# Kernel optimization log

Measured on AMD Instinct MI355X. Metric: run time of the kernel, lower is better.

Reference implementation:

```python
import jax, jax.numpy as jnp
import numpy as np
from jax import lax

WS = 7          # window size
SHIFT = 3       # shift size
HEADS = 16
DIM = 512
NREF = 100
H_IMG = 112
W_IMG = 112
BATCH = 2
HD = DIM // HEADS
SCALE = HD ** (-0.5)
EPS = 1e-5


def _layernorm(x, w, b):
    mu = jnp.mean(x, axis=-1, keepdims=True)
    var = jnp.mean((x - mu) ** 2, axis=-1, keepdims=True)
    return (x - mu) / jnp.sqrt(var + EPS) * w + b


def _rel_pos_index():
    coords = np.stack(np.meshgrid(np.arange(WS), np.arange(WS), indexing='ij'))  # (2,ws,ws)
    cf = coords.reshape(2, -1)
    rel = cf[:, :, None] - cf[:, None, :]
    rel = rel.transpose(1, 2, 0).astype(np.int64)
    rel[..., 0] += WS - 1
    rel[..., 1] += WS - 1
    rel[..., 0] *= 2 * WS - 1
    return rel.sum(-1).reshape(-1)  # (N*N,)

_RPI = _rel_pos_index()


def setup_inputs() -> dict:
    key = jax.random.key(0)
    ks = jax.random.split(key, 16)
    C = DIM
    s = 0.02
    x = jax.random.normal(ks[0], (BATCH, H_IMG * W_IMG, C), jnp.float32)
    x_ref = jax.random.normal(ks[1], (BATCH, NREF, C), jnp.float32)
    # shifted-window attention mask (standard Swin construction)
    img = np.zeros((H_IMG, W_IMG))
    cnt = 0
    for hs in (slice(0, -WS), slice(-WS, -SHIFT), slice(-SHIFT, None)):
        for ws_ in (slice(0, -WS), slice(-WS, -SHIFT), slice(-SHIFT, None)):
            img[hs, ws_] = cnt
            cnt += 1
    mw = img.reshape(H_IMG // WS, WS, W_IMG // WS, WS).transpose(0, 2, 1, 3).reshape(-1, WS * WS)
    am = mw[:, None, :] - mw[:, :, None]
    mask = jnp.asarray(np.where(am != 0, -100.0, 0.0), jnp.float32)  # (nW, N, N)
    return dict(
        x=x, x_ref=x_ref, mask=mask,
        norm1_w=jnp.ones((C,), jnp.float32), norm1_b=jnp.zeros((C,), jnp.float32),
        qkv_w=jax.random.normal(ks[2], (3 * C, C), jnp.float32) * s,
        qkv_b=jnp.zeros((3 * C,), jnp.float32),
        diff_mu=jax.random.normal(ks[3], (1, 1, C), jnp.float32),
        diff_logsigma=jax.random.normal(ks[4], (1, 1, C), jnp.float32) * s,
        rpb_table=jax.random.normal(ks[5], ((2 * WS - 1) ** 2, HEADS), jnp.float32) * s,
        ref_qk_w=jax.random.normal(ks[6], (2 * C, C), jnp.float32) * s,
        ref_qk_b=jnp.zeros((2 * C,), jnp.float32),
        conv_w=jax.random.normal(ks[7], (HEADS, HEADS, 3, 3), jnp.float32) * s,
        conv_b=jnp.zeros((HEADS,), jnp.float32),
        proj_w=jax.random.normal(ks[8], (C, C), jnp.float32) * s,
        proj_b=jnp.zeros((C,), jnp.float32),
        norm2_w=jnp.ones((C,), jnp.float32), norm2_b=jnp.zeros((C,), jnp.float32),
        fc1_w=jax.random.normal(ks[9], (4 * C, C), jnp.float32) * s,
        fc1_b=jnp.zeros((4 * C,), jnp.float32),
        fc2_w=jax.random.normal(ks[10], (C, 4 * C), jnp.float32) * s,
        fc2_b=jnp.zeros((C,), jnp.float32),
        Hh=H_IMG, Ww=W_IMG,
    )


def _window_attention(xw, mask, x_ref, qkv_w, qkv_b, diff_mu, diff_logsigma,
                      rpb_table, ref_qk_w, ref_qk_b, conv_w, conv_b, proj_w, proj_b):
    B_, N, C = xw.shape
    rB = x_ref.shape[0]
    n_win = B_ // rB
    qkv = (xw @ qkv_w.T + qkv_b).reshape(B_, N, 3, HEADS, HD).transpose(2, 0, 3, 1, 4)
    q, k, v = qkv[0], qkv[1], qkv[2]  # (B_, heads, N, hd)
    # reference tokens -> q/v with reparameterized shift/scale
    ref_qk = (x_ref @ ref_qk_w.T + ref_qk_b).reshape(rB, NREF, 2, C).transpose(2, 0, 1, 3)
    ref_q = diff_mu + jnp.exp(diff_logsigma) * ref_qk[0]
    ref_q = ref_q.reshape(rB, NREF, HEADS, HD).transpose(0, 2, 1, 3)
    ref_v = ref_qk[1].reshape(rB, NREF, HEADS, HD).transpose(0, 2, 1, 3)
    ref_k = jnp.repeat(ref_q, n_win, axis=0)  # (B_, heads, nref, hd)
    ref_v = jnp.repeat(ref_v, n_win, axis=0)
    ra = jnp.einsum('bhnd,bhrd->bhnr', q, ref_k)  # (B_, heads, N, nref)
    ra = ra.reshape(rB, n_win, HEADS, N, NREF).transpose(0, 2, 1, 3, 4).reshape(rB, HEADS, n_win * N, NREF)
    # 3 rounds of conv diffusion + layernorm(no affine) + gelu, residual
    for _ in range(3):
        u = lax.conv_general_dilated(ra, conv_w, (1, 1), 'SAME',
                                     dimension_numbers=('NCHW', 'OIHW', 'NCHW'))
        u = u + conv_b[None, :, None, None]
        mu = jnp.mean(u, axis=(-2, -1), keepdims=True)
        var = jnp.mean((u - mu) ** 2, axis=(-2, -1), keepdims=True)
        u = jax.nn.gelu((u - mu) / jnp.sqrt(var + EPS), approximate=False)
        ra = ra + u
    ra = ra.reshape(rB, HEADS, n_win, N, NREF).transpose(0, 2, 1, 3, 4).reshape(B_, HEADS, N, NREF)
    ra = jax.nn.softmax(ra, axis=-1)
    q_new = jnp.einsum('bhnr,bhrd->bhnd', ra, ref_v) * SCALE
    attn = jnp.einsum('bhnd,bhmd->bhnm', q_new, k)
    rpb = rpb_table[_RPI].reshape(N, N, HEADS).transpose(2, 0, 1)  # (heads, N, N)
    attn = attn + rpb[None]
    nW = mask.shape[0]
    attn = attn.reshape(B_ // nW, nW, HEADS, N, N) + mask[None, :, None]
    attn = jax.nn.softmax(attn.reshape(B_, HEADS, N, N), axis=-1)
    out = jnp.einsum('bhnm,bhmd->bhnd', attn, v).transpose(0, 2, 1, 3).reshape(B_, N, C)
    return out @ proj_w.T + proj_b


def reference(x, x_ref, mask, norm1_w, norm1_b, qkv_w, qkv_b, diff_mu, diff_logsigma,
              rpb_table, ref_qk_w, ref_qk_b, conv_w, conv_b, proj_w, proj_b,
              norm2_w, norm2_b, fc1_w, fc1_b, fc2_w, fc2_b, Hh, Ww):
    B, L, C = x.shape
    shortcut = x
    xn = _layernorm(x, norm1_w, norm1_b).reshape(B, Hh, Ww, C)
    # cyclic shift
    sx = jnp.roll(xn, (-SHIFT, -SHIFT), axis=(1, 2))
    # window partition -> (B*nWin, ws*ws, C)
    xw = sx.reshape(B, Hh // WS, WS, Ww // WS, WS, C).transpose(0, 1, 3, 2, 4, 5).reshape(-1, WS * WS, C)
    aw = _window_attention(xw, mask, x_ref, qkv_w, qkv_b, diff_mu, diff_logsigma,
                           rpb_table, ref_qk_w, ref_qk_b, conv_w, conv_b, proj_w, proj_b)
    # window reverse
    sx = aw.reshape(B, Hh // WS, Ww // WS, WS, WS, C).transpose(0, 1, 3, 2, 4, 5).reshape(B, Hh, Ww, C)
    xn = jnp.roll(sx, (SHIFT, SHIFT), axis=(1, 2)).reshape(B, L, C)
    x = shortcut + xn
    h = _layernorm(x, norm2_w, norm2_b)
    h = jax.nn.gelu(h @ fc1_w.T + fc1_b, approximate=False)
    return x + (h @ fc2_w.T + fc2_b)
```

## Files before the change

kernel.cpp:

```cpp
#include <hip/hip_runtime.h>
#include <hip/hip_bf16.h>

typedef __attribute__((ext_vector_type(8))) short short8;
typedef __attribute__((ext_vector_type(8))) unsigned short ushort8;
typedef __attribute__((ext_vector_type(4))) float f32x4;
typedef __attribute__((ext_vector_type(4))) unsigned int u32x4;
typedef __attribute__((ext_vector_type(2))) unsigned int u32x2;

#define DEV __device__ __forceinline__

DEV float gelu_f(float x) { return 0.5f * x * (1.f + erff(x * 0.70710678118654752440f)); }

DEV float bf2f(unsigned short s) {
  unsigned int t = ((unsigned int)s) << 16;
  float f; __builtin_memcpy(&f, &t, 4); return f;
}
DEV unsigned short f2bf(float f) {
  __hip_bfloat16 b = __float2bfloat16(f);
  unsigned short s; __builtin_memcpy(&s, &b, 2); return s;
}

DEV void async_copy16(void* lds, const void* g) {
  __builtin_amdgcn_global_load_lds(
      (const __attribute__((address_space(1))) unsigned int*)g,
      (__attribute__((address_space(3))) unsigned int*)lds, 16, 0, 0);
}

DEV void block_reduce2(float& s, float& s2) {
  __shared__ float red[8];
  int tid = threadIdx.x;
#pragma unroll
  for (int o = 32; o > 0; o >>= 1) { s += __shfl_down(s, o); s2 += __shfl_down(s2, o); }
  if ((tid & 63) == 0) { red[tid >> 6] = s; red[4 + (tid >> 6)] = s2; }
  __syncthreads();
  s  = red[0] + red[1] + red[2] + red[3];
  s2 = red[4] + red[5] + red[6] + red[7];
}

__global__ __launch_bounds__(256) void f2b_all_kernel(
    const float* __restrict__ qkv_w, const float* __restrict__ proj_w,
    const float* __restrict__ fc1_w, const float* __restrict__ fc2_w,
    __hip_bfloat16* __restrict__ wq, __hip_bfloat16* __restrict__ wp,
    __hip_bfloat16* __restrict__ w1, __hip_bfloat16* __restrict__ w2) {
  int i = blockIdx.x * 256 + threadIdx.x;
  const float* src; unsigned short* dst; int o;
  if (i < 98304)       { src = qkv_w;  dst = (unsigned short*)wq; o = i; }
  else if (i < 131072) { src = proj_w; dst = (unsigned short*)wp; o = i - 98304; }
  else if (i < 262144) { src = fc1_w;  dst = (unsigned short*)w1; o = i - 131072; }
  else                 { src = fc2_w;  dst = (unsigned short*)w2; o = i - 262144; }
  f32x4 a = *reinterpret_cast<const f32x4*>(&src[(size_t)o * 8]);
  f32x4 b = *reinterpret_cast<const f32x4*>(&src[(size_t)o * 8 + 4]);
  ushort8 v;
#pragma unroll
  for (int j = 0; j < 4; j++) { v[j] = f2bf(a[j]); v[4 + j] = f2bf(b[j]); }
  *reinterpret_cast<ushort8*>(&dst[(size_t)o * 8]) = v;
}

__global__ __launch_bounds__(256) void maskb_kernel(const float* __restrict__ mask,
                                                    unsigned short* __restrict__ maskB) {
  int i = blockIdx.x * 256 + threadIdx.x;
  int m = i % 56, rest = i / 56;
  int n = rest % 49, win = rest / 49;
  unsigned short v = 0;
  if (m < 49) v = f2bf(mask[((size_t)win * 49 + n) * 49 + m]);
  maskB[i] = v;
}

__global__ __launch_bounds__(256) void rpbt_kernel(const float* __restrict__ rpb,
                                                   unsigned short* __restrict__ rpbT) {
  int i = blockIdx.x * 256 + threadIdx.x;
  if (i >= 43904) return;
  int m = i % 56, rest = i / 56;
  int n = rest % 49, h = rest / 49;
  unsigned short v = 0;
  if (m < 49) {
    int rp = (n / 7 - m / 7 + 6) * 13 + (n % 7 - m % 7 + 6);
    v = f2bf(rpb[rp * 16 + h]);
  }
  rpbT[i] = v;
}

__global__ __launch_bounds__(256) void cwt_kernel(const float* __restrict__ cw,
                                                  unsigned short* __restrict__ cwT) {
  int i = blockIdx.x * 256 + threadIdx.x;
  if (i >= 2560) return;
  int co = i / 160, k = i % 160;
  unsigned short v = 0;
  if (k < 144) {
    int ci = k & 15, p = k >> 4;
    v = f2bf(cw[(co * 16 + ci) * 9 + p]);
  }
  cwT[i] = v;
}

__global__ __launch_bounds__(256) void ln1_window_kernel(
    const float* __restrict__ x, const float* __restrict__ w, const float* __restrict__ b,
    __hip_bfloat16* __restrict__ xw) {
  int tid = threadIdx.x;
  int wave = tid >> 6, lane = tid & 63;
  int t = blockIdx.x * 4 + wave;
  int b_ = t / 49, n = t % 49;
  int bb = b_ >> 8, win = b_ & 255;
  int wi = win >> 4, wj = win & 15;
  int ii = n / 7, jj = n % 7;
  int sh = (wi * 7 + ii + 3) % 112;
  int sw = (wj * 7 + jj + 3) % 112;
  const float* row = x + ((size_t)bb * 12544 + sh * 112 + sw) * 512;
  f32x4 v0 = *reinterpret_cast<const f32x4*>(&row[lane * 8]);
  f32x4 v1 = *reinterpret_cast<const f32x4*>(&row[lane * 8 + 4]);
  float s = 0.f, s2 = 0.f;
#pragma unroll
  for (int j = 0; j < 4; j++) {
    s += v0[j] + v1[j];
    s2 += v0[j] * v0[j] + v1[j] * v1[j];
  }
#pragma unroll
  for (int o = 1; o < 64; o <<= 1) { s += __shfl_xor(s, o); s2 += __shfl_xor(s2, o); }
  float mu = s * (1.f / 512.f);
  float rstd = rsqrtf(s2 * (1.f / 512.f) - mu * mu + 1e-5f);
  f32x4 w0 = *reinterpret_cast<const f32x4*>(&w[lane * 8]);
  f32x4 w1 = *reinterpret_cast<const f32x4*>(&w[lane * 8 + 4]);
  f32x4 c0 = *reinterpret_cast<const f32x4*>(&b[lane * 8]);
  f32x4 c1 = *reinterpret_cast<const f32x4*>(&b[lane * 8 + 4]);
  ushort8 o8;
#pragma unroll
  for (int j = 0; j < 4; j++) {
    o8[j]     = f2bf((v0[j] - mu) * rstd * w0[j] + c0[j]);
    o8[4 + j] = f2bf((v1[j] - mu) * rstd * w1[j] + c1[j]);
  }
  *reinterpret_cast<ushort8*>((unsigned short*)xw + (size_t)t * 512 + lane * 8) = o8;
}

template <int EPI>
__global__ __launch_bounds__(256, 6) void gemm_bt(
    const __hip_bfloat16* __restrict__ A, const __hip_bfloat16* __restrict__ B,
    const float* __restrict__ bias, float* __restrict__ outF,
    __hip_bfloat16* __restrict__ outB, int M, int N, int K) {
  __shared__ __align__(16) __hip_bfloat16 As[64 * 64];
  __shared__ __align__(16) __hip_bfloat16 Bs[128 * 64];
  int nn = N >> 7;
  int nblk = gridDim.x;
  int bid = blockIdx.x;
  int xcd = bid & 7, slot = bid >> 3;
  int q8 = nblk >> 3, r8 = nblk & 7;
  int base = xcd < r8 ? xcd * (q8 + 1) : r8 * (q8 + 1) + (xcd - r8) * q8;
  int lin = base + slot;
  int m0 = (lin / nn) << 6, n0 = (lin % nn) << 7;
  int tid = threadIdx.x;
  int wave = tid >> 6, lane = tid & 63;
  int wr = (wave >> 1) * 32, wc = (wave & 1) * 64;
  int lrow = lane & 15, kq = lane >> 4;
  int srow = lane >> 3, scol = (lane & 7) * 8;
  const __hip_bfloat16* Abase = A + (size_t)m0 * K;
  const __hip_bfloat16* Bbase = B + (size_t)n0 * K;
  f32x4 acc[2][4] = {};
  for (int k0 = 0; k0 < K; k0 += 64) {
#pragma unroll
    for (int i = 0; i < 2; i++) {
      int row = wave * 16 + i * 8;
      async_copy16(&As[row * 64], &Abase[(size_t)(row + srow) * K + k0 + scol]);
    }
#pragma unroll
    for (int i = 0; i < 4; i++) {
      int row = wave * 32 + i * 8;
      async_copy16(&Bs[row * 64], &Bbase[(size_t)(row + srow) * K + k0 + scol]);
    }
    __syncthreads();
#pragma unroll
    for (int ks = 0; ks < 2; ks++) {
      short8 af[2], bf[4];
#pragma unroll
      for (int t = 0; t < 2; t++)
        af[t] = *reinterpret_cast<const short8*>(&As[(wr + t * 16 + lrow) * 64 + ks * 32 + kq * 8]);
#pragma unroll
      for (int t = 0; t < 4; t++)
        bf[t] = *reinterpret_cast<const short8*>(&Bs[(wc + t * 16 + lrow) * 64 + ks * 32 + kq * 8]);
#pragma unroll
      for (int tm = 0; tm < 2; tm++)
#pragma unroll
        for (int tn = 0; tn < 4; tn++)
          acc[tm][tn] = __builtin_amdgcn_mfma_f32_16x16x32_bf16(af[tm], bf[tn], acc[tm][tn], 0, 0, 0);
    }
    __syncthreads();
  }
#pragma unroll
  for (int tm = 0; tm < 2; tm++) {
#pragma unroll
    for (int tn = 0; tn < 4; tn++) {
      int col = n0 + wc + tn * 16 + lrow;
      float bv = bias[col];
#pragma unroll
      for (int r = 0; r < 4; r++) {
        int row = m0 + wr + tm * 16 + kq * 4 + r;
        float v = acc[tm][tn][r] + bv;
        if (EPI == 4) {
          if (col < 512)
            ((unsigned short*)outB)[(size_t)row * 512 + col] = f2bf(v);
          else
            ((unsigned short*)outF)[(size_t)row * 1024 + (col - 512)] = f2bf(v);
        } else {
          size_t o = (size_t)row * N + col;
          if (EPI == 1) outB[o] = __float2bfloat16(v);
          else if (EPI == 2) outB[o] = __float2bfloat16(gelu_f(v));
          else outF[o] += v;
        }
      }
    }
  }
}

__global__ __launch_bounds__(256) void ref_kernel(
    const float* __restrict__ x_ref, const float* __restrict__ w, const float* __restrict__ bias,
    const float* __restrict__ diff_mu, const float* __restrict__ diff_ls,
    unsigned short* __restrict__ refq, unsigned short* __restrict__ refvT) {
  int blk = blockIdx.x;
  int b = blk / 100, r = blk % 100;
  __shared__ float xs[512];
  int tid = threadIdx.x;
  const float* xr = x_ref + (size_t)(b * 100 + r) * 512;
  xs[tid] = xr[tid];
  xs[tid + 256] = xr[tid + 256];
  __syncthreads();
#pragma unroll
  for (int cc = 0; cc < 4; cc++) {
    int c = cc * 256 + tid;
    const float* wr = w + (size_t)c * 512;
    float s = bias[c];
    for (int k = 0; k < 512; k++) s += xs[k] * wr[k];
    if (c < 512) {
      float v = diff_mu[c] + expf(diff_ls[c]) * s;
      int hh = c >> 5, d = c & 31;
      refq[((size_t)(b * 16 + hh) * 100 + r) * 32 + d] = f2bf(v);
    } else {
      int c2 = c - 512, hh = c2 >> 5, d = c2 & 31;
      refvT[(((size_t)b * 16 + hh) * 32 + d) * 128 + r] = f2bf(s);
    }
  }
  if (r < 28) {
#pragma unroll
    for (int j = 0; j < 2; j++) {
      int idx = j * 256 + tid;
      int hh = idx >> 5, d = idx & 31;
      refvT[(((size_t)b * 16 + hh) * 32 + d) * 128 + 100 + r] = 0;
    }
  }
}

__global__ __launch_bounds__(256) void ra_kernel(
    const __hip_bfloat16* __restrict__ q, const unsigned short* __restrict__ refq,
    __hip_bfloat16* __restrict__ ra) {
  __shared__ __align__(16) unsigned short q_s[64 * 40];
  __shared__ __align__(16) unsigned short rq_s[112 * 40];
  int bid = blockIdx.x;
  int blk = (bid & 7) * 1024 + (bid >> 3);
  int b_ = blk >> 4, h = blk & 15;
  int rb = b_ >> 8, win = b_ & 255;
  int tid = threadIdx.x;
  int wave = tid >> 6, lane = tid & 63;
  int lrow = lane & 15, kq = lane >> 4;
  u32x4 z4 = {};
  const unsigned short* qb = (const unsigned short*)q + (size_t)b_ * 49 * 512 + h * 32;
  for (int i = tid; i < 196; i += 256) {
    int n = i >> 2, c = i & 3;
    *reinterpret_cast<u32x4*>(&q_s[n * 40 + c * 8]) =
        *reinterpret_cast<const u32x4*>(&qb[n * 512 + c * 8]);
  }
  for (int i = tid; i < 60; i += 256) {
    int n = 49 + (i >> 2), c = i & 3;
    *reinterpret_cast<u32x4*>(&q_s[n * 40 + c * 8]) = z4;
  }
  const unsigned short* rqg = refq + (size_t)(rb * 16 + h) * 3200;
  for (int i = tid; i < 400; i += 256) {
    int r = i >> 2, c = i & 3;
    *reinterpret_cast<u32x4*>(&rq_s[r * 40 + c * 8]) =
        *reinterpret_cast<const u32x4*>(&rqg[r * 32 + c * 8]);
  }
  for (int i = tid; i < 48; i += 256) {
    int r = 100 + (i >> 2), c = i & 3;
    *reinterpret_cast<u32x4*>(&rq_s[r * 40 + c * 8]) = z4;
  }
  __syncthreads();
  short8 a = *reinterpret_cast<const short8*>(&q_s[(wave * 16 + lrow) * 40 + kq * 8]);
  unsigned short* ra_base = (unsigned short*)ra + ((size_t)(rb * 16 + h) * 12544 + win * 49) * 100;
  f32x4 zero = {};
#pragma unroll
  for (int nt = 0; nt < 7; nt++) {
    short8 b = *reinterpret_cast<const short8*>(&rq_s[(nt * 16 + lrow) * 40 + kq * 8]);
    f32x4 c = __builtin_amdgcn_mfma_f32_16x16x32_bf16(a, b, zero, 0, 0, 0);
    int col = nt * 16 + lrow;
#pragma unroll
    for (int r = 0; r < 4; r++) {
      int n = wave * 16 + kq * 4 + r;
      if (n < 49 && col < 100) ra_base[n * 100 + col] = f2bf(c[r]);
    }
  }
}

DEV int swzi(int pl, int ci) {
  int byte = (pl << 5) + (ci << 1);
  byte ^= ((pl >> 2) & 3) << 4;
  return byte >> 1;
}
__global__ __launch_bounds__(256, 6) void conv_kernel(
    const __hip_bfloat16* __restrict__ ra_, const unsigned short* __restrict__ cwT,
    const float* __restrict__ cb,
    __hip_bfloat16* __restrict__ u_, float* __restrict__ psum, float* __restrict__ psumsq) {
  __shared__ __align__(16) unsigned short in_s[6 * 103 * 16];
  __shared__ __align__(16) unsigned short st_s[4 * 16 * 36];
  __shared__ float sred_s[4][16], sred_s2[4][16];
  const unsigned short* ra = (const unsigned short*)ra_;
  unsigned short* u = (unsigned short*)u_;
  int ytb = blockIdx.x;
  int yt = (ytb & 7) * 392 + (ytb >> 3);
  int bb = blockIdx.y;
  int y0 = yt * 4;
  int tid = threadIdx.x;
  int wave = tid >> 6, lane = tid & 63;
  int lrow = lane & 15, kq = lane >> 4;
  for (int i = tid; i < 288; i += 256) {
    int ci = i & 15, rem = i >> 4;
    int yl = rem / 3, xs = rem % 3;
    int xl = (xs == 0) ? 0 : (100 + xs);
    in_s[swzi(yl * 103 + xl, ci)] = 0;
  }
  if (tid < 192) {
    int unit = tid >> 1, par = tid & 1;
    int ci = unit / 6, yl = unit % 6;
    int gy = y0 - 1 + yl;
    bool rv = (gy >= 0 && gy < 12544);
    const unsigned short* rp = ra + (((size_t)bb * 16 + ci) * 12544 + (rv ? gy : 0)) * 100;
    int plb = yl * 103 + 1;
#pragma unroll 4
    for (int c = par; c < 25; c += 2) {
      u32x2 d = {0u, 0u};
      if (rv) d = *reinterpret_cast<const u32x2*>(&rp[c * 4]);
      int pl = plb + c * 4;
      in_s[swzi(pl + 0, ci)] = (unsigned short)(d[0] & 0xffff);
      in_s[swzi(pl + 1, ci)] = (unsigned short)(d[0] >> 16);
      in_s[swzi(pl + 2, ci)] = (unsigned short)(d[1] & 0xffff);
      in_s[swzi(pl + 3, ci)] = (unsigned short)(d[1] >> 16);
    }
  }
  __syncthreads();

  short8 afr[5];
#pragma unroll
  for (int c = 0; c < 5; c++)
    afr[c] = *reinterpret_cast<const short8*>(&cwT[lrow * 160 + c * 32 + kq * 8]);
  int kqh = kq >> 1, ci0 = (kq & 1) * 8;
  int kyA[5], kxA[5];
#pragma unroll
  for (int c = 0; c < 5; c++) {
    int p = c * 2 + kqh; if (p > 8) p = 0;
    kyA[c] = p / 3; kxA[c] = p % 3;
  }
  float bias_r[4];
#pragma unroll
  for (int r = 0; r < 4; r++) bias_r[r] = cb[kq * 4 + r];
  float s_r[4] = {0.f, 0.f, 0.f, 0.f}, s2_r[4] = {0.f, 0.f, 0.f, 0.f};

  int yl = wave;
  int gy = y0 + yl;
  unsigned short* stw = &st_s[wave * 16 * 36];
  int seg = lane >> 2, part = lane & 3;
  const size_t ubase = ((size_t)bb * 16 * 12544 + gy) * 100;
#pragma unroll
  for (int xp = 0; xp < 4; xp++) {
#pragma unroll
    for (int xh = 0; xh < 2; xh++) {
      int xg = xp * 2 + xh;
      if (xg >= 7) break;
      int px = xg * 16 + lrow;
      int pxc = px < 100 ? px : 99;
      f32x4 acc = {};
#pragma unroll
      for (int c = 0; c < 5; c++) {
        short8 bfrag = *reinterpret_cast<const short8*>(
            &in_s[swzi((yl + kyA[c]) * 103 + pxc + kxA[c], ci0)]);
        acc = __builtin_amdgcn_mfma_f32_16x16x32_bf16(afr[c], bfrag, acc, 0, 0, 0);
      }
      bool valid = px < 100;
#pragma unroll
      for (int r = 0; r < 4; r++) {
        float v = acc[r] + bias_r[r];
        if (valid) {
          stw[(kq * 4 + r) * 36 + xh * 16 + lrow] = f2bf(v);
          s_r[r] += v; s2_r[r] += v * v;
        }
      }
    }
    unsigned short* ug = u + ubase + (size_t)seg * 1254400;
    if (xp < 3) {
      u32x2 d0 = *reinterpret_cast<const u32x2*>(&stw[seg * 36 + part * 4]);
      u32x2 d1 = *reinterpret_cast<const u32x2*>(&stw[seg * 36 + 16 + part * 4]);
      *reinterpret_cast<u32x2*>(&ug[xp * 32 + part * 4]) = d0;
      *reinterpret_cast<u32x2*>(&ug[xp * 32 + 16 + part * 4]) = d1;
    } else if (lane < 16) {
      u32x2 d = *reinterpret_cast<const u32x2*>(&st_s[wave * 16 * 36 + lane * 36]);
      *reinterpret_cast<u32x2*>(&u[ubase + (size_t)lane * 1254400 + 96]) = d;
    }
  }
#pragma unroll
  for (int o = 1; o < 16; o <<= 1)
#pragma unroll
    for (int r = 0; r < 4; r++) { s_r[r] += __shfl_xor(s_r[r], o); s2_r[r] += __shfl_xor(s2_r[r], o); }
  if (lrow == 0)
#pragma unroll
    for (int r = 0; r < 4; r++) { sred_s[wave][kq * 4 + r] = s_r[r]; sred_s2[wave][kq * 4 + r] = s2_r[r]; }
  __syncthreads();
  if (tid < 16) {
    float s  = sred_s[0][tid] + sred_s[1][tid] + sred_s[2][tid] + sred_s[3][tid];
    float s2 = sred_s2[0][tid] + sred_s2[1][tid] + sred_s2[2][tid] + sred_s2[3][tid];
    size_t pi = ((size_t)bb * 3136 + yt) * 16 + tid;
    psum[pi] = s; psumsq[pi] = s2;
  }
}

__global__ __launch_bounds__(256) void conv_stats_kernel(
    const float* __restrict__ psum, const float* __restrict__ psumsq, float* __restrict__ stats) {
  int g = blockIdx.x;
  int bb = g >> 4, co = g & 15;
  int tid = threadIdx.x;
  float s = 0.f, s2 = 0.f;
  for (int t = tid; t < 3136; t += 256) {
    size_t pi = ((size_t)bb * 3136 + t) * 16 + co;
    s += psum[pi];
    s2 += psumsq[pi];
  }
  block_reduce2(s, s2);
  if (tid == 0) {
    const float inv = 1.f / 1254400.f;
    float mu = s * inv;
    float var = s2 * inv - mu * mu;
    stats[g * 2] = mu;
    stats[g * 2 + 1] = rsqrtf(var + 1e-5f);
  }
}

__global__ __launch_bounds__(256) void conv_apply_kernel(
    __hip_bfloat16* __restrict__ ra, const __hip_bfloat16* __restrict__ u,
    const float* __restrict__ stats) {
  const int total8 = 5017600;
  int stride = gridDim.x * 256;
  for (int i = blockIdx.x * 256 + threadIdx.x; i < total8; i += stride) {
    int g = i / 156800;
    float mu = stats[g * 2], rstd = stats[g * 2 + 1];
    ushort8 uu = reinterpret_cast<const ushort8*>(u)[i];
    ushort8 rr = reinterpret_cast<const ushort8*>(ra)[i];
    ushort8 oo;
#pragma unroll
    for (int j = 0; j < 8; j++) {
      float rv = bf2f(rr[j]) + gelu_f((bf2f(uu[j]) - mu) * rstd);
      oo[j] = f2bf(rv);
    }
    reinterpret_cast<ushort8*>(ra)[i] = oo;
  }
}

template <int FUSE>
__global__ __launch_bounds__(256, 8) void attn_kernel(
    const __hip_bfloat16* __restrict__ ra_, const __hip_bfloat16* __restrict__ u_,
    const float* __restrict__ stats, const unsigned short* __restrict__ refvT,
    const __hip_bfloat16* __restrict__ kv_, const unsigned short* __restrict__ rpbT,
    const unsigned short* __restrict__ maskB, __hip_bfloat16* __restrict__ att_) {
  __shared__ __align__(16) char smem[18944];
  unsigned short* P1 = (unsigned short*)smem;
  unsigned short* P2 = (unsigned short*)smem;
  unsigned short* vT = (unsigned short*)(smem + 9216);
  unsigned short* qn = (unsigned short*)(smem + 13824);

#define LSUM(n) (*reinterpret_cast<float*>(&qn[(n) * 40 + 32]))

  int bid = blockIdx.x;
  int blk = (bid & 7) * 1024 + (bid >> 3);
  int b_ = blk >> 4, h = blk & 15;
  int rb = b_ >> 8, win = b_ & 255;
  int tid = threadIdx.x;
  int wave = tid >> 6, lane = tid & 63;
  int lrow = lane & 15, kq = lane >> 4;
  const unsigned short* ra = (const unsigned short*)ra_;
  const unsigned short* ug = (const unsigned short*)u_;
  const unsigned short* kv = (const unsigned short*)kv_;
  unsigned short* att = (unsigned short*)att_;
  u32x2 zz = {};

  if (tid < 64) LSUM(tid) = 1.0f;
  float mu = 0.f, rstd = 0.f;
  if (FUSE) { mu = stats[(rb * 16 + h) * 2]; rstd = stats[(rb * 16 + h) * 2 + 1]; }

  const size_t tile_off = ((size_t)(rb * 16 + h) * 12544 + win * 49) * 100;
  const unsigned short* rab = ra + tile_off;
  const unsigned short* uab = ug + tile_off;
  for (int i = tid; i < 1225; i += 256) {
    int n = i / 25, c = i % 25;
    u32x2 rv = *reinterpret_cast<const u32x2*>(&rab[n * 100 + c * 4]);
    if (FUSE) {
      u32x2 uv = *reinterpret_cast<const u32x2*>(&uab[n * 100 + c * 4]);
      unsigned short rr4[4] = {(unsigned short)(rv[0] & 0xffff), (unsigned short)(rv[0] >> 16),
                               (unsigned short)(rv[1] & 0xffff), (unsigned short)(rv[1] >> 16)};
      unsigned short uu4[4] = {(unsigned short)(uv[0] & 0xffff), (unsigned short)(uv[0] >> 16),
                               (unsigned short)(uv[1] & 0xffff), (unsigned short)(uv[1] >> 16)};
      unsigned short o4[4];
#pragma unroll
      for (int j = 0; j < 4; j++)
        o4[j] = f2bf(bf2f(rr4[j]) + gelu_f((bf2f(uu4[j]) - mu) * rstd));
      u32x2 w;
      w[0] = (unsigned int)o4[0] | ((unsigned int)o4[1] << 16);
      w[1] = (unsigned int)o4[2] | ((unsigned int)o4[3] << 16);
      *reinterpret_cast<u32x2*>(&P1[n * 136 + c * 4]) = w;
    } else {
      *reinterpret_cast<u32x2*>(&P1[n * 136 + c * 4]) = rv;
    }
  }
  for (int i = tid; i < 343; i += 256) {
    int n = i / 7, c = i % 7;
    *reinterpret_cast<u32x2*>(&P1[n * 136 + 100 + c * 4]) = zz;
  }
  __syncthreads();

  if (tid < 196) {
    int n = tid >> 2, q = tid & 3;
    unsigned short* row = P1 + n * 136 + q * 25;
    float e[25];
#pragma unroll
    for (int r = 0; r < 25; r++) e[r] = bf2f(row[r]);
    float mx = -1e30f;
#pragma unroll
    for (int r = 0; r < 25; r++) mx = fmaxf(mx, e[r]);
    mx = fmaxf(mx, __shfl_xor(mx, 1));
    mx = fmaxf(mx, __shfl_xor(mx, 2));
    float sm = 0.f;
#pragma unroll
    for (int r = 0; r < 25; r++) { e[r] = __expf(e[r] - mx); sm += e[r]; }
    sm += __shfl_xor(sm, 1);
    sm += __shfl_xor(sm, 2);
#pragma unroll
    for (int r = 0; r < 25; r++) row[r] = f2bf(e[r]);
    if (q == 0) LSUM(n) = sm;
  }
  __syncthreads();

  const unsigned short* rvtg = refvT + (size_t)(rb * 16 + h) * 4096;
  f32x4 acc1[2] = {};
#pragma unroll
  for (int ks = 0; ks < 4; ks++) {
    short8 a = *reinterpret_cast<const short8*>(&P1[(wave * 16 + lrow) * 136 + ks * 32 + kq * 8]);
#pragma unroll
    for (int dt = 0; dt < 2; dt++) {
      short8 b = *reinterpret_cast<const short8*>(&rvtg[(dt * 16 + lrow) * 128 + ks * 32 + kq * 8]);
      acc1[dt] = __builtin_amdgcn_mfma_f32_16x16x32_bf16(a, b, acc1[dt], 0, 0, 0);
    }
  }
  float invl[4];
#pragma unroll
  for (int r = 0; r < 4; r++)
    invl[r] = 0.17677669529663688f / LSUM(wave * 16 + kq * 4 + r);
#pragma unroll
  for (int dt = 0; dt < 2; dt++)
#pragma unroll
    for (int r = 0; r < 4; r++) {
      int n = wave * 16 + kq * 4 + r;
      qn[n * 40 + dt * 16 + lrow] = f2bf(acc1[dt][r] * invl[r]);
    }
  __syncthreads();

  const unsigned short* kvb = kv + (size_t)b_ * 49 * 1024;
  for (int i = tid; i < 196; i += 256) {
    int m = i >> 2, dg = (i & 3) * 8;
    ushort8 vv = *reinterpret_cast<const ushort8*>(&kvb[m * 1024 + 512 + h * 32 + dg]);
#pragma unroll
    for (int j = 0; j < 8; j++) vT[(dg + j) * 72 + m] = vv[j];
  }
  for (int i = tid; i < 480; i += 256) vT[(i / 15) * 72 + 49 + i % 15] = 0;
  __syncthreads();

  const unsigned short* bt = maskB + (size_t)win * 2744;
  const unsigned short* rt = rpbT + (size_t)h * 2744;
  short8 aq = *reinterpret_cast<const short8*>(&qn[(wave * 16 + lrow) * 40 + kq * 8]);
  f32x4 zero = {};
  float val[4][4];
#pragma unroll
  for (int mt = 0; mt < 4; mt++) {
    int mrow = mt * 16 + lrow;
    int mc = mrow < 49 ? mrow : 48;
    short8 bk = *reinterpret_cast<const short8*>(&kvb[mc * 1024 + h * 32 + kq * 8]);
    f32x4 lg = __builtin_amdgcn_mfma_f32_16x16x32_bf16(aq, bk, zero, 0, 0, 0);
    int m = mrow;
#pragma unroll
    for (int r = 0; r < 4; r++) {
      int n = wave * 16 + kq * 4 + r;
      float v;
      if (m < 49 && n < 49)
        v = lg[r] + bf2f(rt[n * 56 + m]) + bf2f(bt[n * 56 + m]);
      else v = -1e30f;
      val[mt][r] = v;
    }
  }
#pragma unroll
  for (int r = 0; r < 4; r++) {
    float mx = -1e30f;
#pragma unroll
    for (int mt = 0; mt < 4; mt++) mx = fmaxf(mx, val[mt][r]);
    mx = fmaxf(mx, __shfl_xor(mx, 1)); mx = fmaxf(mx, __shfl_xor(mx, 2));
    mx = fmaxf(mx, __shfl_xor(mx, 4)); mx = fmaxf(mx, __shfl_xor(mx, 8));
    float sm = 0.f, e[4];
#pragma unroll
    for (int mt = 0; mt < 4; mt++) { e[mt] = __expf(val[mt][r] - mx); sm += e[mt]; }
    sm += __shfl_xor(sm, 1); sm += __shfl_xor(sm, 2);
    sm += __shfl_xor(sm, 4); sm += __shfl_xor(sm, 8);
    float inv = 1.f / sm;
    int n = wave * 16 + kq * 4 + r;
#pragma unroll
    for (int mt = 0; mt < 4; mt++) P2[n * 72 + mt * 16 + lrow] = f2bf(e[mt] * inv);
  }
  __syncthreads();

  f32x4 acc2[2] = {};
#pragma unroll
  for (int ks = 0; ks < 2; ks++) {
    short8 ap = *reinterpret_cast<const short8*>(&P2[(wave * 16 + lrow) * 72 + ks * 32 + kq * 8]);
#pragma unroll
    for (int dt = 0; dt < 2; dt++) {
      short8 bv = *reinterpret_cast<const short8*>(&vT[(dt * 16 + lrow) * 72 + ks * 32 + kq * 8]);
      acc2[dt] = __builtin_amdgcn_mfma_f32_16x16x32_bf16(ap, bv, acc2[dt], 0, 0, 0);
    }
  }
  unsigned short* ab = att + (size_t)b_ * 49 * 512 + h * 32;
#pragma unroll
  for (int dt = 0; dt < 2; dt++)
#pragma unroll
    for (int r = 0; r < 4; r++) {
      int n = wave * 16 + kq * 4 + r;
      if (n < 49) ab[n * 512 + dt * 16 + lrow] = f2bf(acc2[dt][r]);
    }
#undef LSUM
}

__global__ __launch_bounds__(256) void resid_ln2_kernel(
    const float* __restrict__ x, const __hip_bfloat16* __restrict__ proj_out,
    const float* __restrict__ w2, const float* __restrict__ b2,
    float* __restrict__ out, __hip_bfloat16* __restrict__ hout) {
  int tid = threadIdx.x;
  int wave = tid >> 6, lane = tid & 63;
  int blk = blockIdx.x * 4 + wave;
  int bb = blk / 12544, l = blk % 12544;
  int hh = l / 112, ww = l % 112;
  int hs = (hh + 109) % 112, wsx = (ww + 109) % 112;
  int t = (bb * 256 + (hs / 7) * 16 + (wsx / 7)) * 49 + (hs % 7) * 7 + (wsx % 7);
  const float* xr = x + (size_t)blk * 512 + lane * 8;
  const unsigned short* pr = (const unsigned short*)proj_out + (size_t)t * 512 + lane * 8;
  f32x4 x0 = *reinterpret_cast<const f32x4*>(xr);
  f32x4 x1 = *reinterpret_cast<const f32x4*>(xr + 4);
  ushort8 p8 = *reinterpret_cast<const ushort8*>(pr);
  float v[8];
#pragma unroll
  for (int j = 0; j < 4; j++) {
    v[j]     = x0[j] + bf2f(p8[j]);
    v[4 + j] = x1[j] + bf2f(p8[4 + j]);
  }
  float s = 0.f, s2 = 0.f;
#pragma unroll
  for (int j = 0; j < 8; j++) { s += v[j]; s2 += v[j] * v[j]; }
  float* orow = out + (size_t)blk * 512 + lane * 8;
  f32x4 o0, o1;
#pragma unroll
  for (int j = 0; j < 4; j++) { o0[j] = v[j]; o1[j] = v[4 + j]; }
  *reinterpret_cast<f32x4*>(orow) = o0;
  *reinterpret_cast<f32x4*>(orow + 4) = o1;
#pragma unroll
  for (int o = 1; o < 64; o <<= 1) { s += __shfl_xor(s, o); s2 += __shfl_xor(s2, o); }
  float mu = s * (1.f / 512.f);
  float rstd = rsqrtf(s2 * (1.f / 512.f) - mu * mu + 1e-5f);
  f32x4 w0 = *reinterpret_cast<const f32x4*>(&w2[lane * 8]);
  f32x4 w1 = *reinterpret_cast<const f32x4*>(&w2[lane * 8 + 4]);
  f32x4 c0 = *reinterpret_cast<const f32x4*>(&b2[lane * 8]);
  f32x4 c1 = *reinterpret_cast<const f32x4*>(&b2[lane * 8 + 4]);
  ushort8 h8;
#pragma unroll
  for (int j = 0; j < 4; j++) {
    h8[j]     = f2bf((v[j] - mu) * rstd * w0[j] + c0[j]);
    h8[4 + j] = f2bf((v[4 + j] - mu) * rstd * w1[j] + c1[j]);
  }
  *reinterpret_cast<ushort8*>((unsigned short*)hout + (size_t)blk * 512 + lane * 8) = h8;
}

extern "C" void kernel_launch(void* const* d_in, const int* in_sizes, int n_in,
                              void* d_out, int out_size, void* d_ws, size_t ws_size,
                              hipStream_t stream) {
  const float* x       = (const float*)d_in[0];
  const float* x_ref   = (const float*)d_in[1];
  const float* mask    = (const float*)d_in[2];
  const float* n1w     = (const float*)d_in[3];
  const float* n1b     = (const float*)d_in[4];
  const float* qkv_w   = (const float*)d_in[5];
  const float* qkv_b   = (const float*)d_in[6];
  const float* diff_mu = (const float*)d_in[7];
  const float* diff_ls = (const float*)d_in[8];
  const float* rpb     = (const float*)d_in[9];
  const float* ref_w   = (const float*)d_in[10];
  const float* ref_b   = (const float*)d_in[11];
  const float* conv_w  = (const float*)d_in[12];
  const float* conv_b  = (const float*)d_in[13];
  const float* proj_w  = (const float*)d_in[14];
  const float* proj_b  = (const float*)d_in[15];
  const float* n2w     = (const float*)d_in[16];
  const float* n2b     = (const float*)d_in[17];
  const float* fc1_w   = (const float*)d_in[18];
  const float* fc1_b   = (const float*)d_in[19];
  const float* fc2_w   = (const float*)d_in[20];
  const float* fc2_b   = (const float*)d_in[21];
  float* out = (float*)d_out;

  char* ws = (char*)d_ws;
  size_t off = 0;
  auto alloc = [&](size_t bytes) -> char* {
    char* p = ws + off;
    off += (bytes + 255) & ~(size_t)255;
    return p;
  };
  __hip_bfloat16* wq_bf = (__hip_bfloat16*)alloc(1536ULL * 512 * 2);
  __hip_bfloat16* wp_bf = (__hip_bfloat16*)alloc(512ULL * 512 * 2);
  __hip_bfloat16* w1_bf = (__hip_bfloat16*)alloc(2048ULL * 512 * 2);
  __hip_bfloat16* w2_bf = (__hip_bfloat16*)alloc(512ULL * 2048 * 2);
  unsigned short* refq  = (unsigned short*)alloc(2ULL * 16 * 100 * 32 * 2);
  unsigned short* refvT = (unsigned short*)alloc(2ULL * 16 * 32 * 128 * 2);
  unsigned short* maskB = (unsigned short*)alloc(256ULL * 49 * 56 * 2);
  unsigned short* rpbT  = (unsigned short*)alloc(16ULL * 49 * 56 * 2);
  unsigned short* cwT   = (unsigned short*)alloc(2560ULL * 2);
  float* psum  = (float*)alloc(2ULL * 3136 * 16 * 4);
  float* psumq = (float*)alloc(2ULL * 3136 * 16 * 4);
  float* stats = (float*)alloc(64 * 4);
  char* regX  = alloc(25088ULL * 512 * 2);
  char* regQ  = alloc(25088ULL * 512 * 2);
  char* regRA = alloc(2ULL * 16 * 12544 * 100 * 2);
  char* regU  = alloc(2ULL * 16 * 12544 * 100 * 2);

  __hip_bfloat16* xw_bf   = (__hip_bfloat16*)regX;
  __hip_bfloat16* att_bf  = (__hip_bfloat16*)regX;
  __hip_bfloat16* q_bf    = (__hip_bfloat16*)regQ;
  __hip_bfloat16* h_bf    = (__hip_bfloat16*)regQ;
  __hip_bfloat16* ra      = (__hip_bfloat16*)regRA;
  __hip_bfloat16* hg      = (__hip_bfloat16*)regRA;
  __hip_bfloat16* u       = (__hip_bfloat16*)regU;
  __hip_bfloat16* proj_bf = (__hip_bfloat16*)(regU + 51380224);

  const size_t kv_bytes = 25088ULL * 1024 * 2;
  bool fused = (ws_size >= off + kv_bytes);
  __hip_bfloat16* kv_bf = fused ? (__hip_bfloat16*)alloc(kv_bytes)
                                : (__hip_bfloat16*)regU;

  f2b_all_kernel<<<1536, 256, 0, stream>>>(qkv_w, proj_w, fc1_w, fc2_w,
                                           wq_bf, wp_bf, w1_bf, w2_bf);
  maskb_kernel<<<2744, 256, 0, stream>>>(mask, maskB);
  rpbt_kernel<<<172, 256, 0, stream>>>(rpb, rpbT);
  cwt_kernel<<<10, 256, 0, stream>>>(conv_w, cwT);
  ln1_window_kernel<<<6272, 256, 0, stream>>>(x, n1w, n1b, xw_bf);
  if (fused) {
    gemm_bt<4><<<4704, 256, 0, stream>>>(xw_bf, wq_bf, qkv_b, (float*)kv_bf, q_bf,
                                         25088, 1536, 512);
  } else {
    gemm_bt<1><<<1568, 256, 0, stream>>>(xw_bf, wq_bf, qkv_b, nullptr, q_bf,
                                         25088, 512, 512);
  }
  ref_kernel<<<200, 256, 0, stream>>>(x_ref, ref_w, ref_b, diff_mu, diff_ls, refq, refvT);
  ra_kernel<<<8192, 256, 0, stream>>>(q_bf, refq, ra);
  for (int rd = 0; rd < 3; rd++) {
    conv_kernel<<<dim3(3136, 2), 256, 0, stream>>>(ra, cwT, conv_b, u, psum, psumq);
    conv_stats_kernel<<<32, 256, 0, stream>>>(psum, psumq, stats);
    if (rd < 2 || !fused)
      conv_apply_kernel<<<4096, 256, 0, stream>>>(ra, u, stats);
  }
  if (!fused)
    gemm_bt<1><<<3136, 256, 0, stream>>>(xw_bf, wq_bf + 512 * 512, qkv_b + 512,
                                         nullptr, kv_bf, 25088, 1024, 512);
  if (fused)
    attn_kernel<1><<<8192, 256, 0, stream>>>(ra, u, stats, refvT, kv_bf, rpbT, maskB, att_bf);
  else
    attn_kernel<0><<<8192, 256, 0, stream>>>(ra, u, stats, refvT, kv_bf, rpbT, maskB, att_bf);
  gemm_bt<1><<<1568, 256, 0, stream>>>(att_bf, wp_bf, proj_b, nullptr, proj_bf,
                                       25088, 512, 512);
  resid_ln2_kernel<<<6272, 256, 0, stream>>>(x, proj_bf, n2w, n2b, out, h_bf);
  for (int ch = 0; ch < 2; ch++) {
    const __hip_bfloat16* hA = h_bf + (size_t)ch * 12544 * 512;
    gemm_bt<2><<<3136, 256, 0, stream>>>(hA, w1_bf, fc1_b, nullptr, hg,
                                         12544, 2048, 512);
    gemm_bt<3><<<784, 256, 0, stream>>>(hg, w2_bf, fc2_b,
                                        out + (size_t)ch * 12544 * 512, nullptr,
                                        12544, 512, 2048);
  }
}
```

Baseline: 1.008 ms.

## Fuse conv apply step into next conv round with ping-pong buffers

The separate conv_apply pass (ra += gelu(normalized u)) is folded into the input staging of the following conv_kernel. The updated ra tile is written to a second buffer, and ra/u ping-pong between two buffer pairs so neighbouring tiles read unmodified halo rows. This removes two full read-modify-write passes over the large ra tensor, but needs extra workspace and falls back to the old path when that is unavailable. ra_kernel also drops its LDS staging of the reference queries, loads B fragments straight from global memory, and gets an occupancy hint.

Result: no change. 1.020 ms (+1.1%).

```diff
diff --git a/kernel.cpp b/kernel.cpp
--- a/kernel.cpp
+++ b/kernel.cpp
@@ -246,11 +246,10 @@
   }
 }
 
-__global__ __launch_bounds__(256) void ra_kernel(
+__global__ __launch_bounds__(256, 8) void ra_kernel(
     const __hip_bfloat16* __restrict__ q, const unsigned short* __restrict__ refq,
     __hip_bfloat16* __restrict__ ra) {
   __shared__ __align__(16) unsigned short q_s[64 * 40];
-  __shared__ __align__(16) unsigned short rq_s[112 * 40];
   int bid = blockIdx.x;
   int blk = (bid & 7) * 1024 + (bid >> 3);
   int b_ = blk >> 4, h = blk & 15;
@@ -269,23 +268,16 @@
     int n = 49 + (i >> 2), c = i & 3;
     *reinterpret_cast<u32x4*>(&q_s[n * 40 + c * 8]) = z4;
   }
+  __syncthreads();
+  short8 a = *reinterpret_cast<const short8*>(&q_s[(wave * 16 + lrow) * 40 + kq * 8]);
   const unsigned short* rqg = refq + (size_t)(rb * 16 + h) * 3200;
-  for (int i = tid; i < 400; i += 256) {
-    int r = i >> 2, c = i & 3;
-    *reinterpret_cast<u32x4*>(&rq_s[r * 40 + c * 8]) =
-        *reinterpret_cast<const u32x4*>(&rqg[r * 32 + c * 8]);
-  }
-  for (int i = tid; i < 48; i += 256) {
-    int r = 100 + (i >> 2), c = i & 3;
-    *reinterpret_cast<u32x4*>(&rq_s[r * 40 + c * 8]) = z4;
-  }
-  __syncthreads();
-  short8 a = *reinterpret_cast<const short8*>(&q_s[(wave * 16 + lrow) * 40 + kq * 8]);
   unsigned short* ra_base = (unsigned short*)ra + ((size_t)(rb * 16 + h) * 12544 + win * 49) * 100;
   f32x4 zero = {};
 #pragma unroll
   for (int nt = 0; nt < 7; nt++) {
-    short8 b = *reinterpret_cast<const short8*>(&rq_s[(nt * 16 + lrow) * 40 + kq * 8]);
+    int brow = nt * 16 + lrow;
+    int brc = brow < 100 ? brow : 99;
+    short8 b = *reinterpret_cast<const short8*>(&rqg[brc * 32 + kq * 8]);
     f32x4 c = __builtin_amdgcn_mfma_f32_16x16x32_bf16(a, b, zero, 0, 0, 0);
     int col = nt * 16 + lrow;
 #pragma unroll
@@ -301,14 +293,18 @@
   byte ^= ((pl >> 2) & 3) << 4;
   return byte >> 1;
 }
+template <int APPLY>
 __global__ __launch_bounds__(256, 6) void conv_kernel(
-    const __hip_bfloat16* __restrict__ ra_, const unsigned short* __restrict__ cwT,
-    const float* __restrict__ cb,
+    const __hip_bfloat16* __restrict__ ra_, const __hip_bfloat16* __restrict__ uin_,
+    const float* __restrict__ stats, const unsigned short* __restrict__ cwT,
+    const float* __restrict__ cb, __hip_bfloat16* __restrict__ raout_,
     __hip_bfloat16* __restrict__ u_, float* __restrict__ psum, float* __restrict__ psumsq) {
   __shared__ __align__(16) unsigned short in_s[6 * 103 * 16];
   __shared__ __align__(16) unsigned short st_s[4 * 16 * 36];
   __shared__ float sred_s[4][16], sred_s2[4][16];
   const unsigned short* ra = (const unsigned short*)ra_;
+  const unsigned short* uin = (const unsigned short*)uin_;
+  unsigned short* raout = (unsigned short*)raout_;
   unsigned short* u = (unsigned short*)u_;
   int ytb = blockIdx.x;
   int yt = (ytb & 7) * 392 + (ytb >> 3);
@@ -328,20 +324,57 @@
     int ci = unit / 6, yl = unit % 6;
     int gy = y0 - 1 + yl;
     bool rv = (gy >= 0 && gy < 12544);
-    const unsigned short* rp = ra + (((size_t)bb * 16 + ci) * 12544 + (rv ? gy : 0)) * 100;
+    size_t poff = (((size_t)bb * 16 + ci) * 12544 + (rv ? gy : 0)) * 100;
+    const unsigned short* rp = ra + poff;
+    const unsigned short* up = APPLY ? uin + poff : nullptr;
+    float mu = 0.f, rstd = 0.f;
+    if (APPLY && rv) { mu = stats[(bb * 16 + ci) * 2]; rstd = stats[(bb * 16 + ci) * 2 + 1]; }
     int plb = yl * 103 + 1;
 #pragma unroll 4
     for (int c = par; c < 25; c += 2) {
       u32x2 d = {0u, 0u};
       if (rv) d = *reinterpret_cast<const u32x2*>(&rp[c * 4]);
       int pl = plb + c * 4;
-      in_s[swzi(pl + 0, ci)] = (unsigned short)(d[0] & 0xffff);
-      in_s[swzi(pl + 1, ci)] = (unsigned short)(d[0] >> 16);
-      in_s[swzi(pl + 2, ci)] = (unsigned short)(d[1] & 0xffff);
-      in_s[swzi(pl + 3, ci)] = (unsigned short)(d[1] >> 16);
-    }
-  }
-  __syncthreads();
+      if (APPLY) {
+        u32x2 du = {0u, 0u};
+        if (rv) du = *reinterpret_cast<const u32x2*>(&up[c * 4]);
+        unsigned short rr4[4] = {(unsigned short)(d[0] & 0xffff), (unsigned short)(d[0] >> 16),
+                                 (unsigned short)(d[1] & 0xffff), (unsigned short)(d[1] >> 16)};
+        unsigned short uu4[4] = {(unsigned short)(du[0] & 0xffff), (unsigned short)(du[0] >> 16),
+                                 (unsigned short)(du[1] & 0xffff), (unsigned short)(du[1] >> 16)};
+#pragma unroll
+        for (int j = 0; j < 4; j++) {
+          unsigned short v = 0;
+          if (rv) v = f2bf(bf2f(rr4[j]) + gelu_f((bf2f(uu4[j]) - mu) * rstd));
+          in_s[swzi(pl + j, ci)] = v;
+        }
+      } else {
+        in_s[swzi(pl + 0, ci)] = (unsigned short)(d[0] & 0xffff);
+        in_s[swzi(pl + 1, ci)] = (unsigned short)(d[0] >> 16);
+        in_s[swzi(pl + 2, ci)] = (unsigned short)(d[1] & 0xffff);
+        in_s[swzi(pl + 3, ci)] = (unsigned short)(d[1] >> 16);
+      }
+    }
+  }
+  __syncthreads();
+
+  if (APPLY) {
+    int strip = tid >> 2, part = tid & 3;
+    int ci = strip >> 2, rowl = strip & 3;
+    unsigned short* rout = raout + (((size_t)bb * 16 + ci) * 12544 + (y0 + rowl)) * 100;
+    int pl = (rowl + 1) * 103 + 1;
+    for (int c = part; c < 25; c += 4) {
+      int px = c * 4;
+      unsigned int e0 = in_s[swzi(pl + px + 0, ci)];
+      unsigned int e1 = in_s[swzi(pl + px + 1, ci)];
+      unsigned int e2 = in_s[swzi(pl + px + 2, ci)];
+      unsigned int e3 = in_s[swzi(pl + px + 3, ci)];
+      u32x2 w;
+      w[0] = e0 | (e1 << 16);
+      w[1] = e2 | (e3 << 16);
+      *reinterpret_cast<u32x2*>(&rout[px]) = w;
+    }
+  }
 
   short8 afr[5];
 #pragma unroll
@@ -730,10 +763,11 @@
   float* psum  = (float*)alloc(2ULL * 3136 * 16 * 4);
   float* psumq = (float*)alloc(2ULL * 3136 * 16 * 4);
   float* stats = (float*)alloc(64 * 4);
+  const size_t ra_bytes = 2ULL * 16 * 12544 * 100 * 2;
   char* regX  = alloc(25088ULL * 512 * 2);
   char* regQ  = alloc(25088ULL * 512 * 2);
-  char* regRA = alloc(2ULL * 16 * 12544 * 100 * 2);
-  char* regU  = alloc(2ULL * 16 * 12544 * 100 * 2);
+  char* regRA = alloc(ra_bytes);
+  char* regU  = alloc(ra_bytes);
 
   __hip_bfloat16* xw_bf   = (__hip_bfloat16*)regX;
   __hip_bfloat16* att_bf  = (__hip_bfloat16*)regX;
@@ -745,9 +779,17 @@
   __hip_bfloat16* proj_bf = (__hip_bfloat16*)(regU + 51380224);
 
   const size_t kv_bytes = 25088ULL * 1024 * 2;
-  bool fused = (ws_size >= off + kv_bytes);
+  bool fused = (ws_size >= off + kv_bytes + 256);
   __hip_bfloat16* kv_bf = fused ? (__hip_bfloat16*)alloc(kv_bytes)
                                 : (__hip_bfloat16*)regU;
+
+  bool fused2 = fused && (ws_size >= off + 2 * (ra_bytes + 256));
+  __hip_bfloat16* raB = nullptr;
+  __hip_bfloat16* uB  = nullptr;
+  if (fused2) {
+    raB = (__hip_bfloat16*)alloc(ra_bytes);
+    uB  = (__hip_bfloat16*)alloc(ra_bytes);
+  }
 
   f2b_all_kernel<<<1536, 256, 0, stream>>>(qkv_w, proj_w, fc1_w, fc2_w,
                                            wq_bf, wp_bf, w1_bf, w2_bf);
@@ -764,10 +806,24 @@
   }
   ref_kernel<<<200, 256, 0, stream>>>(x_ref, ref_w, ref_b, diff_mu, diff_ls, refq, refvT);
   ra_kernel<<<8192, 256, 0, stream>>>(q_bf, refq, ra);
-  for (int rd = 0; rd < 3; rd++) {
-    conv_kernel<<<dim3(3136, 2), 256, 0, stream>>>(ra, cwT, conv_b, u, psum, psumq);
+  conv_kernel<0><<<dim3(3136, 2), 256, 0, stream>>>(ra, nullptr, nullptr, cwT, conv_b,
+                                                    nullptr, u, psum, psumq);
+  conv_stats_kernel<<<32, 256, 0, stream>>>(psum, psumq, stats);
+  if (fused2) {
+    conv_kernel<1><<<dim3(3136, 2), 256, 0, stream>>>(ra, u, stats, cwT, conv_b,
+                                                      raB, uB, psum, psumq);
     conv_stats_kernel<<<32, 256, 0, stream>>>(psum, psumq, stats);
-    if (rd < 2 || !fused)
+    conv_kernel<1><<<dim3(3136, 2), 256, 0, stream>>>(raB, uB, stats, cwT, conv_b,
+                                                      ra, u, psum, psumq);
+    conv_stats_kernel<<<32, 256, 0, stream>>>(psum, psumq, stats);
+  } else {
+    for (int rd = 1; rd < 3; rd++) {
+      conv_apply_kernel<<<4096, 256, 0, stream>>>(ra, u, stats);
+      conv_kernel<0><<<dim3(3136, 2), 256, 0, stream>>>(ra, nullptr, nullptr, cwT, conv_b,
+                                                        nullptr, u, psum, psumq);
+      conv_stats_kernel<<<32, 256, 0, stream>>>(psum, psumq, stats);
+    }
+    if (!fused)
       conv_apply_kernel<<<4096, 256, 0, stream>>>(ra, u, stats);
   }
   if (!fused)
```
